# Kernel tuning notes

Measured on AMD Instinct MI355X. Metric: run time of the kernel, lower is better.

## Reference

```python
import jax, jax.numpy as jnp
import numpy as np

U, I, D, E, B = 100000, 50000, 128, 3200000, 4096
KEEP_PROB = 0.8

def setup_inputs() -> dict:
    key = jax.random.key(0)
    ks = jax.random.split(key, 9)
    return {
        "user_emb": 0.01 * jax.random.normal(ks[0], (U, D), dtype=jnp.float32),
        "item_emb": 0.01 * jax.random.normal(ks[1], (I, D), dtype=jnp.float32),
        "vals": jax.random.uniform(ks[2], (E,), dtype=jnp.float32),
        "keep_mask": jax.random.uniform(ks[3], (E,), dtype=jnp.float32),
        "rows": jax.random.randint(ks[4], (E,), 0, U, dtype=jnp.int32),
        "cols": jax.random.randint(ks[5], (E,), 0, I, dtype=jnp.int32),
        "user": jax.random.randint(ks[6], (B,), 0, U, dtype=jnp.int32),
        "pos_item": jax.random.randint(ks[7], (B,), 0, I, dtype=jnp.int32),
        "neg_item": jax.random.randint(ks[8], (B,), 0, I, dtype=jnp.int32),
    }

def reference(user_emb, item_emb, vals, keep_mask, rows, cols, user, pos_item, neg_item):
    # Edge dropout: keep edge iff uniform < keep_prob, rescale by 1/keep_prob.
    # (Equivalent to torch's index filtering, expressed as zeroed values.)
    dvals = jnp.where(keep_mask < KEEP_PROB, vals / KEEP_PROB, 0.0)
    u0, i0 = user_emb, item_emb
    # i_1 = spmm(A^T, u_0): scatter edge messages by item (col) index.  [I, D]
    i1 = jax.ops.segment_sum(dvals[:, None] * u0[rows], cols, num_segments=item_emb.shape[0])
    # u_1 = spmm(A, i_0): scatter edge messages by user (row) index.    [U, D]
    u1 = jax.ops.segment_sum(dvals[:, None] * i0[cols], rows, num_segments=user_emb.shape[0])
    # Layer combination (mean of layer-0 and layer-1), gathered per batch.
    u = (u0[user] + u1[user]) * 0.5        # [B, D]
    i = (i0[pos_item] + i1[pos_item]) * 0.5
    j = (i0[neg_item] + i1[neg_item]) * 0.5
    pos_score = jnp.sum(u * i, axis=1, keepdims=True)  # [B, 1]
    neg_score = jnp.sum(u * j, axis=1, keepdims=True)  # [B, 1]
    return (pos_score, neg_score)
```

## Files before the change

kernel.cpp:

```cpp
#include <hip/hip_runtime.h>

#define DIM 128
#define KEEP_PROB 0.8f
#define UCAP 96
#define ICAP 160
#define SMASK_WORDS 5120
#define CSTRIDE 32

__global__ void slot_kernel(const int* __restrict__ user, const int* __restrict__ pos,
                            const int* __restrict__ neg, int* __restrict__ u_slot,
                            int* __restrict__ i_slot, unsigned* __restrict__ u_mask,
                            unsigned* __restrict__ i_mask, int B) {
    int t = blockIdx.x * blockDim.x + threadIdx.x;
    if (t < B) {
        int u = user[t];
        u_slot[u] = t;
        atomicOr(&u_mask[u >> 5], 1u << (u & 31));
    } else if (t < 2 * B) {
        int it = pos[t - B];
        i_slot[it] = t - B;
        atomicOr(&i_mask[it >> 5], 1u << (it & 31));
    } else if (t < 3 * B) {
        int it = neg[t - 2 * B];
        i_slot[it] = (t - 2 * B) + B;
        atomicOr(&i_mask[it >> 5], 1u << (it & 31));
    }
}

template <bool LDS>
__global__ void fill_bucket_kernel(const float* __restrict__ vals, const float* __restrict__ keep,
                                   const int* __restrict__ rows, const int* __restrict__ cols,
                                   const int* __restrict__ u_slot, const int* __restrict__ i_slot,
                                   const unsigned* __restrict__ masks, int umw, int mw_total,
                                   int* __restrict__ cursor, int2* __restrict__ entries,
                                   int E, int B) {
    __shared__ unsigned sm[LDS ? SMASK_WORDS : 1];
    const unsigned *um, *im;
    if constexpr (LDS) {
        for (int i = threadIdx.x; i < mw_total; i += blockDim.x) sm[i] = masks[i];
        __syncthreads();
        um = sm; im = sm + umw;
    } else {
        um = masks; im = masks + umw;
    }

    int t = blockIdx.x * blockDim.x + threadIdx.x;
    int base = t * 4;
    if (base >= E) return;
    long long ib = (long long)B * UCAP;
    if (base + 3 < E) {
        float4 ka = *(const float4*)(keep + base);
        float4 va = *(const float4*)(vals + base);
        int4 ra = *(const int4*)(rows + base);
        int4 ca = *(const int4*)(cols + base);
        float kk[4] = {ka.x, ka.y, ka.z, ka.w};
        float vv[4] = {va.x, va.y, va.z, va.w};
        int rr[4] = {ra.x, ra.y, ra.z, ra.w};
        int cc[4] = {ca.x, ca.y, ca.z, ca.w};
#pragma unroll
        for (int j = 0; j < 4; j++) {
            if (kk[j] < KEEP_PROB) {
                int r = rr[j], c = cc[j];
                float dv = vv[j] * 1.25f;
                if ((um[r >> 5] >> (r & 31)) & 1u) {
                    int us = u_slot[r];
                    int p = atomicAdd(&cursor[(long long)us * CSTRIDE], 1);
                    if (p < UCAP) entries[(long long)us * UCAP + p] = make_int2(c, __float_as_int(dv));
                }
                if ((im[c >> 5] >> (c & 31)) & 1u) {
                    int is = i_slot[c];
                    int p = atomicAdd(&cursor[(long long)(B + is) * CSTRIDE], 1);
                    if (p < ICAP) entries[ib + (long long)is * ICAP + p] = make_int2(r, __float_as_int(dv));
                }
            }
        }
    } else {
        for (int e = base; e < E; e++) {
            if (keep[e] < KEEP_PROB) {
                int r = rows[e], c = cols[e];
                float dv = vals[e] * 1.25f;
                if ((um[r >> 5] >> (r & 31)) & 1u) {
                    int us = u_slot[r];
                    int p = atomicAdd(&cursor[(long long)us * CSTRIDE], 1);
                    if (p < UCAP) entries[(long long)us * UCAP + p] = make_int2(c, __float_as_int(dv));
                }
                if ((im[c >> 5] >> (c & 31)) & 1u) {
                    int is = i_slot[c];
                    int p = atomicAdd(&cursor[(long long)(B + is) * CSTRIDE], 1);
                    if (p < ICAP) entries[ib + (long long)is * ICAP + p] = make_int2(r, __float_as_int(dv));
                }
            }
        }
    }
}

__global__ void count_kernel(const float* __restrict__ keep, const int* __restrict__ rows,
                             const int* __restrict__ cols, const int* __restrict__ u_slot,
                             const int* __restrict__ i_slot, int* __restrict__ cnt,
                             int E, int B) {
    int t = blockIdx.x * blockDim.x + threadIdx.x;
    int base = t * 4;
    if (base >= E) return;
    for (int e = base; e < base + 4 && e < E; e++) {
        if (keep[e] < KEEP_PROB) {
            int us = u_slot[rows[e]];
            if (us >= 0) atomicAdd(&cnt[us], 1);
            int is = i_slot[cols[e]];
            if (is >= 0) atomicAdd(&cnt[B + is], 1);
        }
    }
}

__global__ void scan_kernel(const int* __restrict__ cnt, int* __restrict__ offs,
                            int* __restrict__ cursor, int n) {
    __shared__ int wave_tot[16];
    __shared__ int carry_s;
    int tid = threadIdx.x, lane = tid & 63, wv = tid >> 6;
    if (tid == 0) carry_s = 0;
    __syncthreads();
    for (int base = 0; base < n; base += 1024) {
        int v = (base + tid < n) ? cnt[base + tid] : 0;
        int x = v;
#pragma unroll
        for (int off = 1; off < 64; off <<= 1) {
            int y = __shfl_up(x, off);
            if (lane >= off) x += y;
        }
        if (lane == 63) wave_tot[wv] = x;
        __syncthreads();
        if (wv == 0 && lane < 16) {
            int tot = wave_tot[lane];
            int s = tot;
#pragma unroll
            for (int off = 1; off < 16; off <<= 1) {
                int y = __shfl_up(s, off);
                if (lane >= off) s += y;
            }
            wave_tot[lane] = s - tot;
        }
        __syncthreads();
        int excl = (x - v) + wave_tot[wv] + carry_s;
        if (base + tid < n) { offs[base + tid] = excl; cursor[base + tid] = excl; }
        __syncthreads();
        if (tid == 1023) carry_s += wave_tot[15] + x;
        __syncthreads();
    }
}

__global__ void fill_csr_kernel(const float* __restrict__ vals, const float* __restrict__ keep,
                                const int* __restrict__ rows, const int* __restrict__ cols,
                                const int* __restrict__ u_slot, const int* __restrict__ i_slot,
                                int* __restrict__ cursor, int2* __restrict__ entries,
                                long long cap, int E, int B) {
    int t = blockIdx.x * blockDim.x + threadIdx.x;
    int base = t * 4;
    if (base >= E) return;
    for (int e = base; e < base + 4 && e < E; e++) {
        if (keep[e] < KEEP_PROB) {
            float dv = vals[e] * 1.25f;
            int us = u_slot[rows[e]];
            if (us >= 0) {
                int p = atomicAdd(&cursor[us], 1);
                if (p < cap) entries[p] = make_int2(cols[e], __float_as_int(dv));
            }
            int is = i_slot[cols[e]];
            if (is >= 0) {
                int p = atomicAdd(&cursor[B + is], 1);
                if (p < cap) entries[p] = make_int2(rows[e], __float_as_int(dv));
            }
        }
    }
}

__global__ void gather_kernel(const int2* __restrict__ entries, const int* __restrict__ offs,
                              const int* __restrict__ cntp, const float* __restrict__ u0,
                              const float* __restrict__ i0, float* __restrict__ u1c,
                              float* __restrict__ i1c, int B, int mode, long long cap) {
    __shared__ float part[3][DIM];
    int wv = threadIdx.x >> 6;
    int lane = threadIdx.x & 63;
    int dest = blockIdx.x;

    const float* table;
    float* dst;
    if (dest < B) { table = i0; dst = u1c + (size_t)dest * DIM; }
    else          { table = u0; dst = i1c + (size_t)(dest - B) * DIM; }

    int n;
    long long base;
    if (mode == 1) {
        n = cntp[(long long)dest * CSTRIDE];
        if (dest < B) { base = (long long)dest * UCAP; if (n > UCAP) n = UCAP; }
        else { base = (long long)B * UCAP + (long long)(dest - B) * ICAP; if (n > ICAP) n = ICAP; }
    } else {
        n = cntp[dest];
        base = offs[dest];
        if (base + (long long)n > cap) { long long rem = cap - base; n = rem < 0 ? 0 : (int)rem; }
    }

    int m = (n - wv + 3) >> 2;
    if (m < 0) m = 0;
    int o = lane * 2;
    float ax = 0.f, ay = 0.f;
    for (int k0 = 0; k0 < m; k0 += 64) {
        int my = k0 + lane;
        int2 e = make_int2(0, 0);
        if (my < m) e = entries[base + wv + 4 * (long long)my];
        int mm = m - k0;
        if (mm > 64) mm = 64;
        int j = 0;
        for (; j + 4 <= mm; j += 4) {
            int s0 = __shfl(e.x, j + 0), s1 = __shfl(e.x, j + 1);
            int s2 = __shfl(e.x, j + 2), s3 = __shfl(e.x, j + 3);
            float d0 = __int_as_float(__shfl(e.y, j + 0));
            float d1 = __int_as_float(__shfl(e.y, j + 1));
            float d2 = __int_as_float(__shfl(e.y, j + 2));
            float d3 = __int_as_float(__shfl(e.y, j + 3));
            float2 r0 = *(const float2*)(table + (size_t)s0 * DIM + o);
            float2 r1 = *(const float2*)(table + (size_t)s1 * DIM + o);
            float2 r2 = *(const float2*)(table + (size_t)s2 * DIM + o);
            float2 r3 = *(const float2*)(table + (size_t)s3 * DIM + o);
            ax += d0 * r0.x; ay += d0 * r0.y;
            ax += d1 * r1.x; ay += d1 * r1.y;
            ax += d2 * r2.x; ay += d2 * r2.y;
            ax += d3 * r3.x; ay += d3 * r3.y;
        }
        for (; j < mm; j++) {
            int s = __shfl(e.x, j);
            float dv = __int_as_float(__shfl(e.y, j));
            float2 r = *(const float2*)(table + (size_t)s * DIM + o);
            ax += dv * r.x; ay += dv * r.y;
        }
    }
    if (wv > 0) { part[wv - 1][o] = ax; part[wv - 1][o + 1] = ay; }
    __syncthreads();
    if (wv == 0) {
        ax += part[0][o] + part[1][o] + part[2][o];
        ay += part[0][o + 1] + part[1][o + 1] + part[2][o + 1];
        *(float2*)(dst + o) = make_float2(ax, ay);
    }
}

__global__ void score_kernel(const float* __restrict__ u0, const float* __restrict__ i0,
                             const float* __restrict__ u1c, const float* __restrict__ i1c,
                             const int* __restrict__ user, const int* __restrict__ pos,
                             const int* __restrict__ neg, const int* __restrict__ u_slot,
                             const int* __restrict__ i_slot, float* __restrict__ out, int B) {
    int wave = (blockIdx.x * blockDim.x + threadIdx.x) >> 6;
    int lane = threadIdx.x & 63;
    if (wave >= B) return;

    int ub = user[wave], pb = pos[wave], nb = neg[wave];
    int usl = u_slot[ub], psl = i_slot[pb], nsl = i_slot[nb];
    int o = lane * 2;

    float2 a0 = *(const float2*)(u0  + (size_t)ub  * DIM + o);
    float2 a1 = *(const float2*)(u1c + (size_t)usl * DIM + o);
    float2 p0 = *(const float2*)(i0  + (size_t)pb  * DIM + o);
    float2 p1 = *(const float2*)(i1c + (size_t)psl * DIM + o);
    float2 n0 = *(const float2*)(i0  + (size_t)nb  * DIM + o);
    float2 n1 = *(const float2*)(i1c + (size_t)nsl * DIM + o);

    float ux = (a0.x + a1.x) * 0.5f, uy = (a0.y + a1.y) * 0.5f;
    float px = (p0.x + p1.x) * 0.5f, py = (p0.y + p1.y) * 0.5f;
    float nx = (n0.x + n1.x) * 0.5f, ny = (n0.y + n1.y) * 0.5f;

    float ps = ux * px + uy * py;
    float ns = ux * nx + uy * ny;
    for (int off = 32; off > 0; off >>= 1) {
        ps += __shfl_down(ps, off);
        ns += __shfl_down(ns, off);
    }
    if (lane == 0) {
        out[wave]     = ps;
        out[B + wave] = ns;
    }
}

extern "C" void kernel_launch(void* const* d_in, const int* in_sizes, int n_in,
                              void* d_out, int out_size, void* d_ws, size_t ws_size,
                              hipStream_t stream) {
    const float* user_emb = (const float*)d_in[0];
    const float* item_emb = (const float*)d_in[1];
    const float* vals     = (const float*)d_in[2];
    const float* keep     = (const float*)d_in[3];
    const int*   rows     = (const int*)d_in[4];
    const int*   cols     = (const int*)d_in[5];
    const int*   user     = (const int*)d_in[6];
    const int*   pos      = (const int*)d_in[7];
    const int*   neg      = (const int*)d_in[8];
    float* out = (float*)d_out;

    int U = in_sizes[0] / DIM;
    int I = in_sizes[1] / DIM;
    int E = in_sizes[2];
    int B = in_sizes[6];

    int umw = ((U + 31) / 32 + 3) & ~3;
    int imw = ((I + 31) / 32 + 3) & ~3;
    int mw_total = umw + imw;

    char* p = (char*)d_ws;
    int* u_slot = (int*)p;              p += (size_t)U * 4;
    int* i_slot = (int*)p;              p += (size_t)I * 4;
    unsigned* u_mask = (unsigned*)p;    p += (size_t)umw * 4;
    unsigned* i_mask = (unsigned*)p;    p += (size_t)imw * 4;
    int* cnt    = (int*)p;              p += (size_t)3 * B * 4;
    int* offs   = (int*)p;              p += (size_t)3 * B * 4;
    int* cursor = (int*)p;              p += (size_t)3 * B * CSTRIDE * 4;
    float* u1c  = (float*)p;            p += (size_t)B * DIM * 4;
    float* i1c  = (float*)p;            p += (size_t)2 * B * DIM * 4;
    int2* entries = (int2*)p;
    size_t used = (size_t)(p - (char*)d_ws);
    long long avail = (long long)ws_size - (long long)used;

    long long bucket_entries = (long long)B * UCAP + (long long)2 * B * ICAP;
    int mode = (avail >= bucket_entries * (long long)sizeof(int2)) ? 1 : 0;

    hipMemsetAsync(u_mask, 0x00,
                   (size_t)(umw + imw + 6 * B + 3 * B * CSTRIDE) * 4, stream);
    if (mode == 0) hipMemsetAsync(u_slot, 0xFF, (size_t)(U + I) * 4, stream);

    slot_kernel<<<(3 * B + 255) / 256, 256, 0, stream>>>(user, pos, neg, u_slot, i_slot,
                                                         u_mask, i_mask, B);

    long long cap;
    if (mode == 1) {
        cap = bucket_entries;
        int fb = ((E + 3) / 4 + 255) / 256;
        if (mw_total <= SMASK_WORDS) {
            fill_bucket_kernel<true><<<fb, 256, 0, stream>>>(vals, keep, rows, cols, u_slot,
                                                             i_slot, u_mask, umw, mw_total,
                                                             cursor, entries, E, B);
        } else {
            fill_bucket_kernel<false><<<fb, 256, 0, stream>>>(vals, keep, rows, cols, u_slot,
                                                              i_slot, u_mask, umw, mw_total,
                                                              cursor, entries, E, B);
        }
        gather_kernel<<<3 * B, 256, 0, stream>>>(entries, offs, cursor, user_emb, item_emb,
                                                 u1c, i1c, B, 1, cap);
    } else {
        cap = avail / (long long)sizeof(int2);
        if (cap < 0) cap = 0;
        int cb = ((E + 3) / 4 + 255) / 256;
        count_kernel<<<cb, 256, 0, stream>>>(keep, rows, cols, u_slot, i_slot, cnt, E, B);
        scan_kernel<<<1, 1024, 0, stream>>>(cnt, offs, cursor, 3 * B);
        fill_csr_kernel<<<cb, 256, 0, stream>>>(vals, keep, rows, cols, u_slot, i_slot,
                                                cursor, entries, cap, E, B);
        gather_kernel<<<3 * B, 256, 0, stream>>>(entries, offs, cnt, user_emb, item_emb,
                                                 u1c, i1c, B, 0, cap);
    }

    score_kernel<<<(B * 64 + 255) / 256, 256, 0, stream>>>(user_emb, item_emb, u1c, i1c,
                                                           user, pos, neg, u_slot, i_slot,
                                                           out, B);
}
```

Before: 218.1 us.

## Bucket edges per node id instead of per batch slot, with a new gather path

Adds a new pipeline that keys edge buckets directly by user and item id through a per-node cursor array, dropping the slot lookup tables. Per-slot counts and offsets are no longer needed. A gather kernel splits each destination's entries across four waves and reduces them in shared memory, and a separate score kernel computes the dot products. It is meant to cut the slot-indirection and counting passes, at the cost of a much larger workspace (U*UCAP + I*ICAP int2 entries) and a memset over U+I cursors. The new path falls back to the old one when the workspace is too small.

```diff
diff --git a/kernel.cpp b/kernel.cpp
--- a/kernel.cpp
+++ b/kernel.cpp
@@ -6,6 +6,198 @@
 #define ICAP 160
 #define SMASK_WORDS 5120
 #define CSTRIDE 32
+
+
+__global__ void mask_kernel(const int* __restrict__ user, const int* __restrict__ pos,
+                            const int* __restrict__ neg, unsigned* __restrict__ u_mask,
+                            unsigned* __restrict__ i_mask, int B) {
+    int t = blockIdx.x * blockDim.x + threadIdx.x;
+    if (t < B) {
+        int u = user[t];
+        atomicOr(&u_mask[u >> 5], 1u << (u & 31));
+    } else if (t < 2 * B) {
+        int it = pos[t - B];
+        atomicOr(&i_mask[it >> 5], 1u << (it & 31));
+    } else if (t < 3 * B) {
+        int it = neg[t - 2 * B];
+        atomicOr(&i_mask[it >> 5], 1u << (it & 31));
+    }
+}
+
+__global__ __launch_bounds__(512)
+void fill2_kernel(const float* __restrict__ vals, const float* __restrict__ keep,
+                  const int* __restrict__ rows, const int* __restrict__ cols,
+                  const unsigned* __restrict__ masks, int umw, int mw_total,
+                  int* __restrict__ cursor, int2* __restrict__ bucketU,
+                  int2* __restrict__ bucketI, int E, int U) {
+    __shared__ unsigned sm[SMASK_WORDS];
+    for (int i = threadIdx.x; i < mw_total; i += blockDim.x) sm[i] = masks[i];
+    __syncthreads();
+    const unsigned* um = sm;
+    const unsigned* im = sm + umw;
+
+    int t = blockIdx.x * blockDim.x + threadIdx.x;
+    int base = t * 4;
+    if (base >= E) return;
+
+    if (base + 3 < E) {
+        float4 ka = *(const float4*)(keep + base);
+        float4 va = *(const float4*)(vals + base);
+        int4 ra = *(const int4*)(rows + base);
+        int4 ca = *(const int4*)(cols + base);
+        float kk[4] = {ka.x, ka.y, ka.z, ka.w};
+        float vv[4] = {va.x, va.y, va.z, va.w};
+        int rr[4] = {ra.x, ra.y, ra.z, ra.w};
+        int cc[4] = {ca.x, ca.y, ca.z, ca.w};
+
+        bool hU[4], hI[4];
+        float dvj[4];
+#pragma unroll
+        for (int j = 0; j < 4; j++) {
+            bool kept = kk[j] < KEEP_PROB;
+            int r = rr[j], c = cc[j];
+            hU[j] = kept && ((um[r >> 5] >> (r & 31)) & 1u);
+            hI[j] = kept && ((im[c >> 5] >> (c & 31)) & 1u);
+            dvj[j] = vv[j] * 1.25f;
+        }
+        int pU[4], pI[4];
+#pragma unroll
+        for (int j = 0; j < 4; j++)
+            pU[j] = hU[j] ? atomicAdd(&cursor[rr[j]], 1) : 0;
+#pragma unroll
+        for (int j = 0; j < 4; j++)
+            pI[j] = hI[j] ? atomicAdd(&cursor[U + cc[j]], 1) : 0;
+#pragma unroll
+        for (int j = 0; j < 4; j++)
+            if (hU[j] && pU[j] < UCAP)
+                bucketU[(long long)rr[j] * UCAP + pU[j]] =
+                    make_int2(cc[j], __float_as_int(dvj[j]));
+#pragma unroll
+        for (int j = 0; j < 4; j++)
+            if (hI[j] && pI[j] < ICAP)
+                bucketI[(long long)cc[j] * ICAP + pI[j]] =
+                    make_int2(rr[j], __float_as_int(dvj[j]));
+    } else {
+        for (int e = base; e < E; e++) {
+            if (keep[e] < KEEP_PROB) {
+                int r = rows[e], c = cols[e];
+                float dv = vals[e] * 1.25f;
+                if ((um[r >> 5] >> (r & 31)) & 1u) {
+                    int p = atomicAdd(&cursor[r], 1);
+                    if (p < UCAP) bucketU[(long long)r * UCAP + p] = make_int2(c, __float_as_int(dv));
+                }
+                if ((im[c >> 5] >> (c & 31)) & 1u) {
+                    int p = atomicAdd(&cursor[U + c], 1);
+                    if (p < ICAP) bucketI[(long long)c * ICAP + p] = make_int2(r, __float_as_int(dv));
+                }
+            }
+        }
+    }
+}
+
+__global__ void gather2_kernel(const int2* __restrict__ bucketU, const int2* __restrict__ bucketI,
+                               const int* __restrict__ cursor, const int* __restrict__ user,
+                               const int* __restrict__ pos, const int* __restrict__ neg,
+                               const float* __restrict__ u0, const float* __restrict__ i0,
+                               float* __restrict__ u1c, float* __restrict__ i1c, int B, int U) {
+    __shared__ float part[3][DIM];
+    int wv = threadIdx.x >> 6;
+    int lane = threadIdx.x & 63;
+    int dest = blockIdx.x;
+
+    const float* table;
+    float* dst;
+    const int2* ent;
+    long long base;
+    int n;
+    if (dest < B) {
+        int id = user[dest];
+        table = i0; dst = u1c + (size_t)dest * DIM;
+        n = cursor[id]; if (n > UCAP) n = UCAP;
+        ent = bucketU; base = (long long)id * UCAP;
+    } else {
+        int id = (dest < 2 * B) ? pos[dest - B] : neg[dest - 2 * B];
+        table = u0; dst = i1c + (size_t)(dest - B) * DIM;
+        n = cursor[U + id]; if (n > ICAP) n = ICAP;
+        ent = bucketI; base = (long long)id * ICAP;
+    }
+
+    int m = (n - wv + 3) >> 2;
+    if (m < 0) m = 0;
+    int o = lane * 2;
+    float ax = 0.f, ay = 0.f;
+    for (int k0 = 0; k0 < m; k0 += 64) {
+        int my = k0 + lane;
+        int2 e = make_int2(0, 0);
+        if (my < m) e = ent[base + wv + 4 * (long long)my];
+        int mm = m - k0;
+        if (mm > 64) mm = 64;
+        int j = 0;
+        for (; j + 4 <= mm; j += 4) {
+            int s0 = __shfl(e.x, j + 0), s1 = __shfl(e.x, j + 1);
+            int s2 = __shfl(e.x, j + 2), s3 = __shfl(e.x, j + 3);
+            float d0 = __int_as_float(__shfl(e.y, j + 0));
+            float d1 = __int_as_float(__shfl(e.y, j + 1));
+            float d2 = __int_as_float(__shfl(e.y, j + 2));
+            float d3 = __int_as_float(__shfl(e.y, j + 3));
+            float2 r0 = *(const float2*)(table + (size_t)s0 * DIM + o);
+            float2 r1 = *(const float2*)(table + (size_t)s1 * DIM + o);
+            float2 r2 = *(const float2*)(table + (size_t)s2 * DIM + o);
+            float2 r3 = *(const float2*)(table + (size_t)s3 * DIM + o);
+            ax += d0 * r0.x; ay += d0 * r0.y;
+            ax += d1 * r1.x; ay += d1 * r1.y;
+            ax += d2 * r2.x; ay += d2 * r2.y;
+            ax += d3 * r3.x; ay += d3 * r3.y;
+        }
+        for (; j < mm; j++) {
+            int s = __shfl(e.x, j);
+            float dv = __int_as_float(__shfl(e.y, j));
+            float2 r = *(const float2*)(table + (size_t)s * DIM + o);
+            ax += dv * r.x; ay += dv * r.y;
+        }
+    }
+    if (wv > 0) { part[wv - 1][o] = ax; part[wv - 1][o + 1] = ay; }
+    __syncthreads();
+    if (wv == 0) {
+        ax += part[0][o] + part[1][o] + part[2][o];
+        ay += part[0][o + 1] + part[1][o + 1] + part[2][o + 1];
+        *(float2*)(dst + o) = make_float2(ax, ay);
+    }
+}
+
+__global__ void score2_kernel(const float* __restrict__ u0, const float* __restrict__ i0,
+                              const float* __restrict__ u1c, const float* __restrict__ i1c,
+                              const int* __restrict__ user, const int* __restrict__ pos,
+                              const int* __restrict__ neg, float* __restrict__ out, int B) {
+    int wave = (blockIdx.x * blockDim.x + threadIdx.x) >> 6;
+    int lane = threadIdx.x & 63;
+    if (wave >= B) return;
+
+    int ub = user[wave], pb = pos[wave], nb = neg[wave];
+    int o = lane * 2;
+
+    float2 a0 = *(const float2*)(u0  + (size_t)ub * DIM + o);
+    float2 a1 = *(const float2*)(u1c + (size_t)wave * DIM + o);
+    float2 p0 = *(const float2*)(i0  + (size_t)pb * DIM + o);
+    float2 p1 = *(const float2*)(i1c + (size_t)wave * DIM + o);
+    float2 n0 = *(const float2*)(i0  + (size_t)nb * DIM + o);
+    float2 n1 = *(const float2*)(i1c + (size_t)(B + wave) * DIM + o);
+
+    float ux = (a0.x + a1.x) * 0.5f, uy = (a0.y + a1.y) * 0.5f;
+    float px = (p0.x + p1.x) * 0.5f, py = (p0.y + p1.y) * 0.5f;
+    float nx = (n0.x + n1.x) * 0.5f, ny = (n0.y + n1.y) * 0.5f;
+
+    float ps = ux * px + uy * py;
+    float ns = ux * nx + uy * ny;
+    for (int off = 32; off > 0; off >>= 1) {
+        ps += __shfl_down(ps, off);
+        ns += __shfl_down(ns, off);
+    }
+    if (lane == 0) {
+        out[wave]     = ps;
+        out[B + wave] = ns;
+    }
+}
 
 __global__ void slot_kernel(const int* __restrict__ user, const int* __restrict__ pos,
                             const int* __restrict__ neg, int* __restrict__ u_slot,
@@ -300,6 +492,35 @@
     int imw = ((I + 31) / 32 + 3) & ~3;
     int mw_total = umw + imw;
 
+    {
+        char* p2 = (char*)d_ws;
+        unsigned* u_mask2 = (unsigned*)p2;  p2 += (size_t)umw * 4;
+        unsigned* i_mask2 = (unsigned*)p2;  p2 += (size_t)imw * 4;
+        int* cursor2 = (int*)p2;            p2 += (size_t)(U + I) * 4;
+        float* u1c2  = (float*)p2;          p2 += (size_t)B * DIM * 4;
+        float* i1c2  = (float*)p2;          p2 += (size_t)2 * B * DIM * 4;
+        int2* bucketU = (int2*)p2;          p2 += (size_t)U * UCAP * 8;
+        int2* bucketI = (int2*)p2;          p2 += (size_t)I * ICAP * 8;
+        size_t need2 = (size_t)(p2 - (char*)d_ws);
+
+        if (ws_size >= need2 && mw_total <= SMASK_WORDS) {
+            hipMemsetAsync(u_mask2, 0x00, (size_t)(umw + imw + U + I) * 4, stream);
+            mask_kernel<<<(3 * B + 255) / 256, 256, 0, stream>>>(user, pos, neg,
+                                                                 u_mask2, i_mask2, B);
+            int fb = ((E + 3) / 4 + 511) / 512;
+            fill2_kernel<<<fb, 512, 0, stream>>>(vals, keep, rows, cols, u_mask2,
+                                                 umw, mw_total, cursor2,
+                                                 bucketU, bucketI, E, U);
+            gather2_kernel<<<3 * B, 256, 0, stream>>>(bucketU, bucketI, cursor2,
+                                                      user, pos, neg, user_emb, item_emb,
+                                                      u1c2, i1c2, B, U);
+            score2_kernel<<<(B * 64 + 255) / 256, 256, 0, stream>>>(user_emb, item_emb,
+                                                                    u1c2, i1c2, user, pos,
+                                                                    neg, out, B);
+            return;
+        }
+    }
+
     char* p = (char*)d_ws;
     int* u_slot = (int*)p;              p += (size_t)U * 4;
     int* i_slot = (int*)p;              p += (size_t)I * 4;
```

Result: no change. 216.1 us (-0.9%).
